# Kernel optimization log

Hardware: AMD Instinct MI355X
Metric: run time of the kernel (lower is better)

## Reference

```python
import jax, jax.numpy as jnp
import numpy as np

B, T, D = 64, 4096, 256
UNITS = 256

def setup_inputs() -> dict:
    key = jax.random.key(0)
    k0, k1, k2, k3 = jax.random.split(key, 4)
    lstm_output = jax.random.normal(k0, (B, T, D), dtype=jnp.float32)
    # Glorot-ish scaled dense weights (no bias per module)
    W1 = jax.random.normal(k1, (D, UNITS), dtype=jnp.float32) * (1.0 / np.sqrt(D))
    W2 = jax.random.normal(k2, (D, UNITS), dtype=jnp.float32) * (1.0 / np.sqrt(D))
    v = jax.random.normal(k3, (UNITS, 1), dtype=jnp.float32) * (1.0 / np.sqrt(UNITS))
    return {"lstm_output": lstm_output, "W1": W1, "W2": W2, "v": v}

def reference(lstm_output, W1, W2, v):
    # query/key: [B, T, units]
    query = jnp.einsum("btd,du->btu", lstm_output, W1)
    key = jnp.einsum("btd,du->btu", lstm_output, W2)
    # score: [B, T, 1]
    score = jnp.einsum("btu,uo->bto", jnp.tanh(query + key), v)
    # softmax over time axis (axis=1)
    attention_weights = jax.nn.softmax(score, axis=1)
    # context: [B, D]
    context_vector = jnp.sum(attention_weights * lstm_output, axis=1)
    return (context_vector, attention_weights)
```

## Files before the change

kernel.cpp:

```cpp
#include <hip/hip_runtime.h>
#include <math.h>

#define B 64
#define T 4096
#define D 256
#define U 256

typedef __attribute__((ext_vector_type(8)))  short s16x8;
typedef __attribute__((ext_vector_type(16))) float f32x16;

#define MT 32
#define SPB 16
#define NBLK ((B*T)/(MT*SPB))
#define LDAP 33

#define TCH 128
#define NCH (T / TCH)

#define DPP_ADD(v, ctrl)                                                     \
  v += __int_as_float(__builtin_amdgcn_update_dpp(                           \
      0, __float_as_int(v), ctrl, 0xF, 0xF, true))

__global__ __launch_bounds__(512, 2) void scores_mfma_kernel(
    const float* __restrict__ A,
    const float* __restrict__ W1,
    const float* __restrict__ W2,
    const float* __restrict__ v,
    float* __restrict__ s_out)
{
  __shared__ uint4 AH[32 * LDAP];
  __shared__ uint4 AL[32 * LDAP];
  __shared__ float red[32][8];

  const int tid  = threadIdx.x;
  const int lane = tid & 63;
  const int wv   = tid >> 6;
  const int l31  = lane & 31;
  const int half = lane >> 5;

  const int n = wv * 32 + l31;
  s16x8 Bh[16], Bl[16];
#pragma unroll
  for (int s = 0; s < 16; ++s) {
    s16x8 bh, bl;
#pragma unroll
    for (int j = 0; j < 8; ++j) {
      const int k = s * 16 + half * 8 + j;
      const float w = W1[k * 256 + n] + W2[k * 256 + n];
      const unsigned int uw = __float_as_uint(w);
      const float wl = w - __uint_as_float(uw & 0xffff0000u);
      bh[j] = (short)(uw >> 16);
      bl[j] = (short)(__float_as_uint(wl) >> 16);
    }
    Bh[s] = bh; Bl[s] = bl;
  }
  const float vv = v[n];

  const int sm  = tid >> 4;
  const int sc0 = tid & 15;

  const size_t row0 = (size_t)blockIdx.x * (MT * SPB);
  float4 rg[4];
  {
    const float4* src = (const float4*)(A + (row0 + sm) * 256);
#pragma unroll
    for (int i = 0; i < 4; ++i) rg[i] = src[sc0 + 16 * i];
  }

  for (int step = 0; step < SPB; ++step) {
    const size_t rowbase = row0 + (size_t)step * MT;

#pragma unroll
    for (int i = 0; i < 4; ++i) {
      const float4 a = rg[i];
      const int k  = 4 * (sc0 + 16 * i);
      const int k8 = k >> 3;
      const int off = (k >> 2) & 1;
      const unsigned int ux = __float_as_uint(a.x), uy = __float_as_uint(a.y);
      const unsigned int uz = __float_as_uint(a.z), uw = __float_as_uint(a.w);
      const uint2 hi2 = make_uint2((ux >> 16) | (uy & 0xffff0000u),
                                   (uz >> 16) | (uw & 0xffff0000u));
      const float lx = a.x - __uint_as_float(ux & 0xffff0000u);
      const float ly = a.y - __uint_as_float(uy & 0xffff0000u);
      const float lz = a.z - __uint_as_float(uz & 0xffff0000u);
      const float lw = a.w - __uint_as_float(uw & 0xffff0000u);
      const uint2 lo2 = make_uint2(
          (__float_as_uint(lx) >> 16) | (__float_as_uint(ly) & 0xffff0000u),
          (__float_as_uint(lz) >> 16) | (__float_as_uint(lw) & 0xffff0000u));
      ((uint2*)&AH[k8 * LDAP + sm])[off] = hi2;
      ((uint2*)&AL[k8 * LDAP + sm])[off] = lo2;
    }
    __syncthreads();

    if (step + 1 < SPB) {
      const float4* src = (const float4*)(A + (rowbase + MT + sm) * 256);
#pragma unroll
      for (int i = 0; i < 4; ++i) rg[i] = src[sc0 + 16 * i];
    }

    f32x16 a0 = {}, a1 = {}, a2 = {};
#pragma unroll
    for (int s = 0; s < 16; ++s) {
      const uint4 qh = AH[(2 * s + half) * LDAP + l31];
      const uint4 ql = AL[(2 * s + half) * LDAP + l31];
      const s16x8 ah = __builtin_bit_cast(s16x8, qh);
      const s16x8 al = __builtin_bit_cast(s16x8, ql);
      a0 = __builtin_amdgcn_mfma_f32_32x32x16_bf16(ah, Bh[s], a0, 0, 0, 0);
      a1 = __builtin_amdgcn_mfma_f32_32x32x16_bf16(ah, Bl[s], a1, 0, 0, 0);
      a2 = __builtin_amdgcn_mfma_f32_32x32x16_bf16(al, Bh[s], a2, 0, 0, 0);
    }

#pragma unroll
    for (int r = 0; r < 16; ++r) {
      const float x = a0[r] + a1[r] + a2[r];
      const float e = __expf(x + x);
      float p = (1.f - 2.f * __builtin_amdgcn_rcpf(e + 1.f)) * vv;
      DPP_ADD(p, 0xB1);
      DPP_ADD(p, 0x4E);
      DPP_ADD(p, 0x141);
      DPP_ADD(p, 0x140);
      p += __int_as_float(
          __builtin_amdgcn_ds_swizzle(__float_as_int(p), 0x401F));
      if (l31 == 0)
        red[(r & 3) + 8 * (r >> 2) + 4 * half][wv] = p;
    }
    __syncthreads();

    if (tid < 32) {
      const float4* rp = (const float4*)&red[tid][0];
      const float4 ra = rp[0], rb = rp[1];
      s_out[rowbase + tid] = ra.x + ra.y + ra.z + ra.w + rb.x + rb.y + rb.z + rb.w;
    }
  }
}

__global__ __launch_bounds__(1024) void softmax_kernel(float* __restrict__ attn) {
    const int b = blockIdx.x;
    float* row = attn + (long)b * T;
    const int tid = threadIdx.x;
    const int wave = tid >> 6, lane = tid & 63;

    __shared__ float lmax[16];
    __shared__ float lsum[16];
    __shared__ float bcast[2];

    float4 s = ((const float4*)row)[tid];
    float m = fmaxf(fmaxf(s.x, s.y), fmaxf(s.z, s.w));
    for (int off = 32; off > 0; off >>= 1) m = fmaxf(m, __shfl_down(m, off));
    if (lane == 0) lmax[wave] = m;
    __syncthreads();
    if (tid == 0) {
        float mm = lmax[0];
        for (int i = 1; i < 16; ++i) mm = fmaxf(mm, lmax[i]);
        bcast[0] = mm;
    }
    __syncthreads();
    m = bcast[0];

    float4 e;
    e.x = expf(s.x - m); e.y = expf(s.y - m);
    e.z = expf(s.z - m); e.w = expf(s.w - m);
    float sum = e.x + e.y + e.z + e.w;
    for (int off = 32; off > 0; off >>= 1) sum += __shfl_down(sum, off);
    if (lane == 0) lsum[wave] = sum;
    __syncthreads();
    if (tid == 0) {
        float ss = 0.f;
        for (int i = 0; i < 16; ++i) ss += lsum[i];
        bcast[1] = 1.0f / ss;
    }
    __syncthreads();
    const float inv = bcast[1];
    e.x *= inv; e.y *= inv; e.z *= inv; e.w *= inv;
    ((float4*)row)[tid] = e;
}

__global__ __launch_bounds__(256, 4) void context_partial_kernel(
    const float* __restrict__ A, const float* __restrict__ attn,
    float* __restrict__ part)
{
    const int chunk = blockIdx.x;
    const int b = blockIdx.y;
    const int tg = threadIdx.x >> 6;
    const int l = threadIdx.x & 63;
    const int dl = l * 4;
    const long tokbase = (long)b * T + (long)chunk * TCH + (long)tg * 32;

    const float4* wp = (const float4*)(attn + tokbase);
    float4 acc = make_float4(0.f, 0.f, 0.f, 0.f);
#pragma unroll
    for (int t8 = 0; t8 < 32; t8 += 8) {
        const float4 wa = wp[t8 / 4];
        const float4 wb = wp[t8 / 4 + 1];
        float w[8];
        *(float4*)&w[0] = wa;
        *(float4*)&w[4] = wb;
#pragma unroll
        for (int j = 0; j < 8; ++j) {
            const float4 x = *(const float4*)(A + (tokbase + t8 + j) * 256 + dl);
            acc.x = fmaf(w[j], x.x, acc.x);
            acc.y = fmaf(w[j], x.y, acc.y);
            acc.z = fmaf(w[j], x.z, acc.z);
            acc.w = fmaf(w[j], x.w, acc.w);
        }
    }

    __shared__ float4 red[4][64];
    red[tg][l] = acc;
    __syncthreads();
    if (tg == 0) {
        float4 r = red[0][l];
        const float4 r1 = red[1][l], r2 = red[2][l], r3 = red[3][l];
        r.x += r1.x + r2.x + r3.x;
        r.y += r1.y + r2.y + r3.y;
        r.z += r1.z + r2.z + r3.z;
        r.w += r1.w + r2.w + r3.w;
        float* p = part + ((long)chunk * B + b) * D + dl;
        p[0] = r.x; p[1] = r.y; p[2] = r.z; p[3] = r.w;
    }
}

__global__ void context_reduce_kernel(const float* __restrict__ part,
                                      float* __restrict__ ctx) {
    const int i = blockIdx.x * 256 + threadIdx.x;
    float s = 0.f;
    for (int c = 0; c < NCH; ++c) s += part[(long)c * (B * D) + i];
    ctx[i] = s;
}

extern "C" void kernel_launch(void* const* d_in, const int* in_sizes, int n_in,
                              void* d_out, int out_size, void* d_ws, size_t ws_size,
                              hipStream_t stream) {
    const float* lstm = (const float*)d_in[0];
    const float* W1   = (const float*)d_in[1];
    const float* W2   = (const float*)d_in[2];
    const float* v    = (const float*)d_in[3];

    float* out  = (float*)d_out;
    float* ctx  = out;
    float* attn = out + B * D;

    float* part = (float*)d_ws;

    scores_mfma_kernel<<<NBLK, 512, 0, stream>>>(lstm, W1, W2, v, attn);
    softmax_kernel<<<B, 1024, 0, stream>>>(attn);
    context_partial_kernel<<<dim3(NCH, B), 256, 0, stream>>>(lstm, attn, part);
    context_reduce_kernel<<<(B * D) / 256, 256, 0, stream>>>(part, ctx);
}
```

Measured before the change: 443.9 us.

## Replace block reductions with atomics and double-buffer LDS in scores kernel

The scores kernel now double-buffers the bf16 split tiles in LDS, which removes the second __syncthreads per step. The per-wave partial score sums go straight to global memory through atomicAdd instead of an LDS reduction. The context step merges the partial and reduce kernels into one kernel that atomically accumulates into the output, and a zero-fill kernel runs first to clear it. This trades barriers and a kernel launch for global atomic traffic and float summation order that is no longer deterministic.

```diff
diff --git a/kernel.cpp b/kernel.cpp
--- a/kernel.cpp
+++ b/kernel.cpp
@@ -20,6 +20,12 @@
 #define DPP_ADD(v, ctrl)                                                     \
   v += __int_as_float(__builtin_amdgcn_update_dpp(                           \
       0, __float_as_int(v), ctrl, 0xF, 0xF, true))
+
+__global__ __launch_bounds__(256) void zero_out_kernel(float4* __restrict__ p,
+                                                       int n4) {
+  const int i = blockIdx.x * 256 + threadIdx.x;
+  if (i < n4) p[i] = make_float4(0.f, 0.f, 0.f, 0.f);
+}
 
 __global__ __launch_bounds__(512, 2) void scores_mfma_kernel(
     const float* __restrict__ A,
@@ -28,9 +34,8 @@
     const float* __restrict__ v,
     float* __restrict__ s_out)
 {
-  __shared__ uint4 AH[32 * LDAP];
-  __shared__ uint4 AL[32 * LDAP];
-  __shared__ float red[32][8];
+  __shared__ uint4 AH[2][32 * LDAP];
+  __shared__ uint4 AL[2][32 * LDAP];
 
   const int tid  = threadIdx.x;
   const int lane = tid & 63;
@@ -67,6 +72,7 @@
     for (int i = 0; i < 4; ++i) rg[i] = src[sc0 + 16 * i];
   }
 
+  int buf = 0;
   for (int step = 0; step < SPB; ++step) {
     const size_t rowbase = row0 + (size_t)step * MT;
 
@@ -87,8 +93,8 @@
       const uint2 lo2 = make_uint2(
           (__float_as_uint(lx) >> 16) | (__float_as_uint(ly) & 0xffff0000u),
           (__float_as_uint(lz) >> 16) | (__float_as_uint(lw) & 0xffff0000u));
-      ((uint2*)&AH[k8 * LDAP + sm])[off] = hi2;
-      ((uint2*)&AL[k8 * LDAP + sm])[off] = lo2;
+      ((uint2*)&AH[buf][k8 * LDAP + sm])[off] = hi2;
+      ((uint2*)&AL[buf][k8 * LDAP + sm])[off] = lo2;
     }
     __syncthreads();
 
@@ -101,8 +107,8 @@
     f32x16 a0 = {}, a1 = {}, a2 = {};
 #pragma unroll
     for (int s = 0; s < 16; ++s) {
-      const uint4 qh = AH[(2 * s + half) * LDAP + l31];
-      const uint4 ql = AL[(2 * s + half) * LDAP + l31];
+      const uint4 qh = AH[buf][(2 * s + half) * LDAP + l31];
+      const uint4 ql = AL[buf][(2 * s + half) * LDAP + l31];
       const s16x8 ah = __builtin_bit_cast(s16x8, qh);
       const s16x8 al = __builtin_bit_cast(s16x8, ql);
       a0 = __builtin_amdgcn_mfma_f32_32x32x16_bf16(ah, Bh[s], a0, 0, 0, 0);
@@ -122,15 +128,10 @@
       p += __int_as_float(
           __builtin_amdgcn_ds_swizzle(__float_as_int(p), 0x401F));
       if (l31 == 0)
-        red[(r & 3) + 8 * (r >> 2) + 4 * half][wv] = p;
-    }
-    __syncthreads();
-
-    if (tid < 32) {
-      const float4* rp = (const float4*)&red[tid][0];
-      const float4 ra = rp[0], rb = rp[1];
-      s_out[rowbase + tid] = ra.x + ra.y + ra.z + ra.w + rb.x + rb.y + rb.z + rb.w;
-    }
+        atomicAdd(&s_out[rowbase + (r & 3) + 8 * (r >> 2) + 4 * half], p);
+    }
+
+    buf ^= 1;
   }
 }
 
@@ -175,9 +176,9 @@
     ((float4*)row)[tid] = e;
 }
 
-__global__ __launch_bounds__(256, 4) void context_partial_kernel(
+__global__ __launch_bounds__(256, 8) void context_kernel(
     const float* __restrict__ A, const float* __restrict__ attn,
-    float* __restrict__ part)
+    float* __restrict__ ctx)
 {
     const int chunk = blockIdx.x;
     const int b = blockIdx.y;
@@ -215,17 +216,12 @@
         r.y += r1.y + r2.y + r3.y;
         r.z += r1.z + r2.z + r3.z;
         r.w += r1.w + r2.w + r3.w;
-        float* p = part + ((long)chunk * B + b) * D + dl;
-        p[0] = r.x; p[1] = r.y; p[2] = r.z; p[3] = r.w;
-    }
-}
-
-__global__ void context_reduce_kernel(const float* __restrict__ part,
-                                      float* __restrict__ ctx) {
-    const int i = blockIdx.x * 256 + threadIdx.x;
-    float s = 0.f;
-    for (int c = 0; c < NCH; ++c) s += part[(long)c * (B * D) + i];
-    ctx[i] = s;
+        float* p = ctx + b * D + dl;
+        atomicAdd(p + 0, r.x);
+        atomicAdd(p + 1, r.y);
+        atomicAdd(p + 2, r.z);
+        atomicAdd(p + 3, r.w);
+    }
 }
 
 extern "C" void kernel_launch(void* const* d_in, const int* in_sizes, int n_in,
@@ -240,10 +236,10 @@
     float* ctx  = out;
     float* attn = out + B * D;
 
-    float* part = (float*)d_ws;
+    const int n4 = (B * D + B * T) / 4;
+    zero_out_kernel<<<(n4 + 255) / 256, 256, 0, stream>>>((float4*)out, n4);
 
     scores_mfma_kernel<<<NBLK, 512, 0, stream>>>(lstm, W1, W2, v, attn);
     softmax_kernel<<<B, 1024, 0, stream>>>(attn);
-    context_partial_kernel<<<dim3(NCH, B), 256, 0, stream>>>(lstm, attn, part);
-    context_reduce_kernel<<<(B * D) / 256, 256, 0, stream>>>(part, ctx);
-}
+    context_kernel<<<dim3(NCH, B), 256, 0, stream>>>(lstm, attn, ctx);
+}
```

After: 466.4 us. 5.1% more time.
